# Kernel tuning notes

Measured on AMD Instinct MI355X. Metric: run time of the kernel, lower is better.

Reference implementation:

```python
import jax, jax.numpy as jnp
import numpy as np
import math

B, L, D, H = 2, 2048, 1024, 16
HD = D // H  # 64
SYNC_THRESHOLD = -0.7
LN_EPS = 1e-12


def setup_inputs() -> dict:
    key = jax.random.key(0)
    ks = jax.random.split(key, 12)
    s = 0.02
    return {
        "hidden_states": jax.random.normal(ks[0], (B, L, D), dtype=jnp.float32),
        "attention_mask": jnp.zeros((B, 1, 1, L), dtype=jnp.float32),
        "phi": jax.random.normal(ks[1], (B, L, H), dtype=jnp.float32),
        "Wq": jax.random.normal(ks[2], (D, D), dtype=jnp.float32) * s,
        "bq": jnp.zeros((D,), dtype=jnp.float32),
        "Wk": jax.random.normal(ks[3], (D, D), dtype=jnp.float32) * s,
        "bk": jnp.zeros((D,), dtype=jnp.float32),
        "Wv": jax.random.normal(ks[4], (D, D), dtype=jnp.float32) * s,
        "bv": jnp.zeros((D,), dtype=jnp.float32),
        "Wo": jax.random.normal(ks[5], (D, D), dtype=jnp.float32) * s,
        "bo": jnp.zeros((D,), dtype=jnp.float32),
        "ln_g": jnp.ones((D,), dtype=jnp.float32),
        "ln_b": jnp.zeros((D,), dtype=jnp.float32),
    }


def _shape(x):  # [B,L,D] -> [B,H,L,HD]
    return x.reshape(B, L, H, HD).transpose(0, 2, 1, 3)


def _rotate_half(x):
    x1, x2 = jnp.split(x, 2, axis=-1)
    return jnp.concatenate([-x2, x1], axis=-1)


def reference(hidden_states, attention_mask, phi, Wq, bq, Wk, bk, Wv, bv, Wo, bo, ln_g, ln_b):
    residual = hidden_states
    q = _shape(hidden_states @ Wq.T + bq)
    k = _shape(hidden_states @ Wk.T + bk)
    v = _shape(hidden_states @ Wv.T + bv)

    # phase per (batch, head, token): [B,H,L,1]; constant across head_dim,
    # so cos/sin of the concatenated phase are the same scalar per token/head.
    p = jnp.transpose(phi, (0, 2, 1))[..., None]
    cos_p = jnp.cos(p)
    sin_p = jnp.sin(p)
    q_rot = q * cos_p + _rotate_half(q) * sin_p
    k_rot = k * cos_p + _rotate_half(k) * sin_p

    scores = jnp.einsum("bhqd,bhkd->bhqk", q_rot, k_rot) / math.sqrt(HD)

    # data-dependent sync mask: mask pairs whose phase difference is anti-synced
    delta_phi = p - jnp.swapaxes(p, -1, -2)           # [B,H,L,L]
    eye = jnp.eye(L, dtype=bool)[None, None]          # [1,1,L,L]
    sync_mask = (jnp.cos(delta_phi) < SYNC_THRESHOLD) & ~eye
    scores = jnp.where(sync_mask, -1e9, scores)
    scores = scores + attention_mask

    # all-masked edge case: zero diagonal score so softmax attends to self
    row_max = jnp.max(scores, axis=-1, keepdims=True)
    all_masked = row_max <= -1e8
    scores = jnp.where(all_masked & eye, 0.0, scores)

    probs = jax.nn.softmax(scores, axis=-1)
    ctx = jnp.einsum("bhqk,bhkd->bhqd", probs, v)
    ctx = ctx.transpose(0, 2, 1, 3).reshape(B, L, D)

    out = ctx @ Wo.T + bo
    x = out + residual
    mean = jnp.mean(x, axis=-1, keepdims=True)
    var = jnp.var(x, axis=-1, keepdims=True)
    return (x - mean) / jnp.sqrt(var + LN_EPS) * ln_g + ln_b
```

## Files before the change

### kernel.cpp

```cpp
#include <hip/hip_runtime.h>
#include <cmath>

#define BB 2
#define LL 2048
#define DD 1024
#define HH 16
#define HDD 64

typedef _Float16 v8h __attribute__((ext_vector_type(8)));
typedef _Float16 v4h __attribute__((ext_vector_type(4)));
typedef _Float16 v2h __attribute__((ext_vector_type(2)));
typedef float v4f __attribute__((ext_vector_type(4)));

#define LOG2E 1.44269504089f
#define NEGB  (-1.442695e9f)

#define GLD(gp, lp)                                                        \
  __builtin_amdgcn_global_load_lds(                                        \
      (const __attribute__((address_space(1))) void*)(gp),                 \
      (__attribute__((address_space(3))) void*)(lp), 16, 0, 0)

__global__ __launch_bounds__(256) void cvt_all(
    const float* __restrict__ hs, const float* __restrict__ wq,
    const float* __restrict__ wk, const float* __restrict__ wv,
    const float* __restrict__ wo, _Float16* __restrict__ hsh,
    _Float16* __restrict__ wqkvh, _Float16* __restrict__ woh)
{
  const int i = blockIdx.x * 256 + threadIdx.x;
  const float* s;
  _Float16* d;
  if (i < 1048576)      { s = hs + (size_t)i * 4;            d = hsh + (size_t)i * 4; }
  else if (i < 1310720) { int j = i - 1048576; s = wq + (size_t)j * 4; d = wqkvh + (size_t)j * 4; }
  else if (i < 1572864) { int j = i - 1310720; s = wk + (size_t)j * 4; d = wqkvh + 1048576 + (size_t)j * 4; }
  else if (i < 1835008) { int j = i - 1572864; s = wv + (size_t)j * 4; d = wqkvh + 2097152 + (size_t)j * 4; }
  else                  { int j = i - 1835008; s = wo + (size_t)j * 4; d = woh + (size_t)j * 4; }
  float4 v = *(const float4*)s;
  v4h o;
  o[0] = (_Float16)v.x; o[1] = (_Float16)v.y;
  o[2] = (_Float16)v.z; o[3] = (_Float16)v.w;
  *(v4h*)d = o;
}

__global__ __launch_bounds__(256) void csgen(
    const float* __restrict__ phi, const float* __restrict__ amk,
    unsigned* __restrict__ csh2, float* __restrict__ aml2)
{
  const int o = blockIdx.x * 256 + threadIdx.x;
  if (o < BB * LL) aml2[o] = amk[o] * LOG2E;
  const int l = o & 2047;
  const int h = (o >> 11) & 15;
  const int b = o >> 15;
  const float ph = phi[(b * 2048 + l) * 16 + h];
  v2h cs;
  cs[0] = (_Float16)cosf(ph);
  cs[1] = (_Float16)sinf(ph);
  csh2[o] = __builtin_bit_cast(unsigned, cs);
}

__device__ __forceinline__ void gemm_loop(
    const _Float16* __restrict__ A, const _Float16* __restrict__ W, const int K,
    const int m0, const int n0, const int tid, const int wave, const int lane,
    _Float16* As, _Float16* Bs, v4f acc[4][4])
{
  const int quad = lane >> 4;
  const int ql = lane & 15;
  const int wm = (wave >> 1) * 64;
  const int wn = (wave & 1) * 64;
  const int srow = tid >> 2;
  const int skof = (tid & 3) * 8;
  const _Float16* Ap = A + (size_t)(m0 + srow) * K + skof;
  const _Float16* Wp = W + (size_t)(n0 + srow) * K + skof;
  const size_t rstep = (size_t)64 * K;
  for (int k0 = 0; k0 < K; k0 += 32) {
    __syncthreads();
    GLD(Ap + k0,         As + tid * 8);
    GLD(Ap + rstep + k0, As + 2048 + tid * 8);
    GLD(Wp + k0,         Bs + tid * 8);
    GLD(Wp + rstep + k0, Bs + 2048 + tid * 8);
    __syncthreads();
    v8h af[4], bf[4];
#pragma unroll
    for (int mt = 0; mt < 4; ++mt)
      af[mt] = *(const v8h*)&As[(wm + mt * 16 + ql) * 32 + quad * 8];
#pragma unroll
    for (int nt = 0; nt < 4; ++nt)
      bf[nt] = *(const v8h*)&Bs[(wn + nt * 16 + ql) * 32 + quad * 8];
#pragma unroll
    for (int mt = 0; mt < 4; ++mt)
#pragma unroll
      for (int nt = 0; nt < 4; ++nt)
        acc[mt][nt] = __builtin_amdgcn_mfma_f32_16x16x32_f16(
            af[mt], bf[nt], acc[mt][nt], 0, 0, 0);
  }
}

__global__ __launch_bounds__(256) void gemm_qkv(
    const _Float16* __restrict__ A, const _Float16* __restrict__ W,
    const float* __restrict__ bqp, const float* __restrict__ bkp,
    const float* __restrict__ bvp, const unsigned* __restrict__ csh2,
    _Float16* __restrict__ qh, _Float16* __restrict__ kh,
    _Float16* __restrict__ vt2)
{
  __shared__ _Float16 As[128 * 32];
  __shared__ _Float16 Bs[128 * 32];
  const int tid = threadIdx.x, lane = tid & 63, wave = tid >> 6;
  const int quad = lane >> 4, ql = lane & 15;
  const int m0 = blockIdx.y * 128, n0 = blockIdx.x * 128;
  v4f acc[4][4];
#pragma unroll
  for (int mt = 0; mt < 4; ++mt)
#pragma unroll
    for (int nt = 0; nt < 4; ++nt) acc[mt][nt] = (v4f){0.f, 0.f, 0.f, 0.f};
  gemm_loop(A, W, DD, m0, n0, tid, wave, lane, As, Bs, acc);

  const int buf = n0 >> 10;
  const int col0 = (n0 & 1023) + (wave & 1) * 64;
  const int hh = col0 >> 6;
  const int mr0 = m0 + (wave >> 1) * 64;

  if (buf == 2) {
    float bb4[4];
#pragma unroll
    for (int nt = 0; nt < 4; ++nt) bb4[nt] = bvp[col0 + nt * 16 + ql];
#pragma unroll
    for (int mt = 0; mt < 4; ++mt) {
      const int row = mr0 + mt * 16 + quad * 4;
      const int b_ = row >> 11;
      const int l = row & 2047;
      _Float16* dst = vt2 + ((size_t)(b_ * 16 + hh) * 32 + (l >> 6)) * 4096 +
                      ((l >> 2) & 15) * 256;
#pragma unroll
      for (int nt = 0; nt < 4; ++nt) {
        const int d = nt * 16 + ql;
        v4h o4;
#pragma unroll
        for (int r = 0; r < 4; ++r) o4[r] = (_Float16)(acc[mt][nt][r] + bb4[nt]);
        *(v4h*)&dst[d * 4] = o4;
      }
    }
  } else {
    const float scl = (buf == 0) ? 0.125f * LOG2E : 1.0f;
    _Float16* outp = (buf == 0) ? qh : kh;
    const float* bias = (buf == 0) ? bqp : bkp;
    float bb4[4];
#pragma unroll
    for (int nt = 0; nt < 4; ++nt) bb4[nt] = bias[col0 + nt * 16 + ql];
#pragma unroll
    for (int mt = 0; mt < 4; ++mt)
#pragma unroll
      for (int r = 0; r < 4; ++r) {
        const int row = mr0 + mt * 16 + quad * 4 + r;
        const int b_ = row >> 11;
        const int l = row & 2047;
        const v2h c2 = __builtin_bit_cast(
            v2h, csh2[(b_ * 16 + hh) * 2048 + l]);
        const float c = (float)c2[0], s = (float)c2[1];
        _Float16* orow = outp + (size_t)row * DD + col0 + ql;
#pragma unroll
        for (int pp = 0; pp < 2; ++pp) {
          const float a0 = acc[mt][pp][r] + bb4[pp];
          const float a1 = acc[mt][pp + 2][r] + bb4[pp + 2];
          orow[pp * 16]        = (_Float16)((a0 * c - a1 * s) * scl);
          orow[(pp + 2) * 16]  = (_Float16)((a1 * c + a0 * s) * scl);
        }
      }
  }
}

__global__ __launch_bounds__(256) void gemm_o(
    const _Float16* __restrict__ A, const _Float16* __restrict__ W,
    const float* __restrict__ bo, const float* __restrict__ res,
    float* __restrict__ out)
{
  __shared__ _Float16 As[128 * 32];
  __shared__ _Float16 Bs[64 * 32];
  const int tid = threadIdx.x, lane = tid & 63, wave = tid >> 6;
  const int quad = lane >> 4, ql = lane & 15;
  const int m0 = blockIdx.y * 128, n0 = blockIdx.x * 64;
  v4f acc[4][2];
#pragma unroll
  for (int mt = 0; mt < 4; ++mt)
#pragma unroll
    for (int nt = 0; nt < 2; ++nt) acc[mt][nt] = (v4f){0.f, 0.f, 0.f, 0.f};
  const int wm = (wave >> 1) * 64;
  const int wn = (wave & 1) * 32;
  const int srow = tid >> 2;
  const int skof = (tid & 3) * 8;
  const _Float16* Ap = A + (size_t)(m0 + srow) * DD + skof;
  const _Float16* Wp = W + (size_t)(n0 + srow) * DD + skof;
  const size_t rstep = (size_t)64 * DD;
  for (int k0 = 0; k0 < DD; k0 += 32) {
    __syncthreads();
    GLD(Ap + k0,         As + tid * 8);
    GLD(Ap + rstep + k0, As + 2048 + tid * 8);
    GLD(Wp + k0,         Bs + tid * 8);
    __syncthreads();
    v8h af[4], bf[2];
#pragma unroll
    for (int mt = 0; mt < 4; ++mt)
      af[mt] = *(const v8h*)&As[(wm + mt * 16 + ql) * 32 + quad * 8];
#pragma unroll
    for (int nt = 0; nt < 2; ++nt)
      bf[nt] = *(const v8h*)&Bs[(wn + nt * 16 + ql) * 32 + quad * 8];
#pragma unroll
    for (int mt = 0; mt < 4; ++mt)
#pragma unroll
      for (int nt = 0; nt < 2; ++nt)
        acc[mt][nt] = __builtin_amdgcn_mfma_f32_16x16x32_f16(
            af[mt], bf[nt], acc[mt][nt], 0, 0, 0);
  }
#pragma unroll
  for (int nt = 0; nt < 2; ++nt) {
    const int col = n0 + wn + nt * 16 + ql;
    const float bb = bo[col];
#pragma unroll
    for (int mt = 0; mt < 4; ++mt)
#pragma unroll
      for (int r = 0; r < 4; ++r) {
        const int row = m0 + wm + mt * 16 + quad * 4 + r;
        const size_t ix = (size_t)row * DD + col;
        out[ix] = acc[mt][nt][r] + bb + res[ix];
      }
  }
}

__global__ __launch_bounds__(256) void attn_db(
    const _Float16* __restrict__ Q, const _Float16* __restrict__ K,
    const _Float16* __restrict__ VT2, const unsigned* __restrict__ csh2,
    const float* __restrict__ aml2, _Float16* __restrict__ ctx)
{
  __shared__ _Float16 Kt[2][4096];
  __shared__ _Float16 Vt[2][4096];
  __shared__ float amL[LL];

  const int tid  = threadIdx.x;
  const int lane = tid & 63;
  const int wave = tid >> 6;
  const int quad = lane >> 4;
  const int ql   = lane & 15;
  const int bid  = blockIdx.x;
  const int bh = bid & 31;
  const int qt = bid >> 5;
  const int h  = bh & 15;
  const int b  = bh >> 4;
  const int q0w = qt * 64 + wave * 16;
  const int qglob = q0w + ql;
  const int csb = bh * LL;

  {
    const float* amb = aml2 + b * LL;
    for (int i = tid; i < LL; i += 256) amL[i] = amb[i];
  }

  v8h qf[2];
  {
    const _Float16* qp = Q + ((size_t)(b * LL + qglob)) * DD + h * 64 + quad * 8;
    qf[0] = *(const v8h*)qp;
    qf[1] = *(const v8h*)(qp + 32);
  }
  v4h bq = (v4h){0, 0, 0, 0};
  {
    const v2h c2 = __builtin_bit_cast(v2h, csh2[csb + qglob]);
    if (quad == 0) { bq[0] = c2[0]; bq[1] = c2[1]; }
  }
  const v4h ones = (v4h){(_Float16)1.f, (_Float16)1.f,
                         (_Float16)1.f, (_Float16)1.f};

  v4f o[4];
#pragma unroll
  for (int nt = 0; nt < 4; ++nt) o[nt] = (v4f){0.f, 0.f, 0.f, 0.f};
  v4f lacc = (v4f){0.f, 0.f, 0.f, 0.f};

  const _Float16* Kb   = K + (size_t)(b * LL) * DD + h * 64;
  const _Float16* VTb2 = VT2 + (size_t)bh * 131072;
  const unsigned* csk = csh2 + csb;

  const int srow = tid >> 3;
  const int kch  = (tid & 7) ^ (srow & 7);

  {
    const size_t kg = (size_t)srow * 1024 + kch * 8;
    GLD(Kb + kg,             &Kt[0][tid * 8]);
    GLD(Kb + kg + 32 * 1024, &Kt[0][2048 + tid * 8]);
    GLD(VTb2 + tid * 8,          &Vt[0][tid * 8]);
    GLD(VTb2 + 2048 + tid * 8,   &Vt[0][2048 + tid * 8]);
  }
  unsigned cs_cur[4], cs_nxt[4];
#pragma unroll
  for (int c = 0; c < 4; ++c) cs_cur[c] = csk[c * 16 + ql];
  __syncthreads();

  for (int t = 0; t < 32; ++t) {
    const int k0 = t * 64;
    const int buf = t & 1;
    if (t < 31) {
      const int k1 = k0 + 64;
      const size_t kg = (size_t)(k1 + srow) * 1024 + kch * 8;
      GLD(Kb + kg,             &Kt[buf ^ 1][tid * 8]);
      GLD(Kb + kg + 32 * 1024, &Kt[buf ^ 1][2048 + tid * 8]);
      const _Float16* vsrc = VTb2 + (size_t)(t + 1) * 4096;
      GLD(vsrc + tid * 8,        &Vt[buf ^ 1][tid * 8]);
      GLD(vsrc + 2048 + tid * 8, &Vt[buf ^ 1][2048 + tid * 8]);
#pragma unroll
      for (int c = 0; c < 4; ++c) cs_nxt[c] = csk[k1 + c * 16 + ql];
    }
    const _Float16* KtB = Kt[buf];
    const _Float16* VtB = Vt[buf];

    v4f st[4], dd[4];
#pragma unroll
    for (int c = 0; c < 4; ++c) {
      const int row = c * 16 + ql;
      const int sw = row & 7;
      v8h a0 = *(const v8h*)&KtB[row * 64 + ((quad ^ sw) << 3)];
      v8h a1 = *(const v8h*)&KtB[row * 64 + (((quad + 4) ^ sw) << 3)];
      v4f z = *(const v4f*)&amL[k0 + c * 16 + quad * 4];
      z = __builtin_amdgcn_mfma_f32_16x16x32_f16(a0, qf[0], z, 0, 0, 0);
      z = __builtin_amdgcn_mfma_f32_16x16x32_f16(a1, qf[1], z, 0, 0, 0);
      st[c] = z;
      const v2h c2 = __builtin_bit_cast(v2h, cs_cur[c]);
      v4h a = (v4h){0, 0, 0, 0};
      if (quad == 0) { a[0] = c2[0]; a[1] = c2[1]; }
      dd[c] = __builtin_amdgcn_mfma_f32_16x16x16f16(
          a, bq, (v4f){0.f, 0.f, 0.f, 0.f}, 0, 0, 0);
    }

    v4h pf[4];
#pragma unroll
    for (int c = 0; c < 4; ++c) {
      float p[4];
#pragma unroll
      for (int r = 0; r < 4; ++r)
        p[r] = __builtin_amdgcn_exp2f((dd[c][r] < -0.7f) ? NEGB : st[c][r]);
      const unsigned u01 = __builtin_bit_cast(
          unsigned, __builtin_amdgcn_cvt_pkrtz(p[0], p[1]));
      const unsigned u23 = __builtin_bit_cast(
          unsigned, __builtin_amdgcn_cvt_pkrtz(p[2], p[3]));
      pf[c] = __builtin_bit_cast(v4h, make_uint2(u01, u23));
    }

#pragma unroll
    for (int c = 0; c < 4; ++c) {
      lacc = __builtin_amdgcn_mfma_f32_16x16x16f16(pf[c], ones, lacc, 0, 0, 0);
#pragma unroll
      for (int nt = 0; nt < 4; ++nt) {
        const v4h vv = *(const v4h*)&VtB[((c * 4 + quad) * 64 +
                                          nt * 16 + ql) * 4];
        o[nt] = __builtin_amdgcn_mfma_f32_16x16x16f16(pf[c], vv, o[nt], 0, 0, 0);
      }
    }
#pragma unroll
    for (int c = 0; c < 4; ++c) cs_cur[c] = cs_nxt[c];
    __syncthreads();
  }

#pragma unroll
  for (int r = 0; r < 4; ++r) {
    const int q = q0w + quad * 4 + r;
    const float lr = lacc[r];
    const size_t ob = (size_t)(b * LL + q) * DD + h * 64 + ql;
    if (lr <= 0.f) {
      const _Float16* vsrc = VTb2 + (q >> 6) * 4096 +
                             ((q >> 2) & 15) * 256 + (q & 3);
#pragma unroll
      for (int nt = 0; nt < 4; ++nt)
        ctx[ob + nt * 16] = vsrc[(nt * 16 + ql) * 4];
    } else {
      const float inv = 1.f / lr;
      ctx[ob + 0]  = (_Float16)(o[0][r] * inv);
      ctx[ob + 16] = (_Float16)(o[1][r] * inv);
      ctx[ob + 32] = (_Float16)(o[2][r] * inv);
      ctx[ob + 48] = (_Float16)(o[3][r] * inv);
    }
  }
}

__global__ __launch_bounds__(256) void layernorm(
    const float* __restrict__ x, const float* __restrict__ g,
    const float* __restrict__ bta, float* __restrict__ out)
{
  __shared__ float red[8];
  const int row = blockIdx.x;
  const int tid = threadIdx.x;
  const float* xr = x + (size_t)row * DD;
  float lsum = 0.f, lsq = 0.f;
  float v[4];
#pragma unroll
  for (int i = 0; i < 4; ++i) {
    v[i] = xr[tid + i * 256];
    lsum += v[i];
    lsq += v[i] * v[i];
  }
#pragma unroll
  for (int off = 32; off > 0; off >>= 1) {
    lsum += __shfl_down(lsum, off, 64);
    lsq  += __shfl_down(lsq,  off, 64);
  }
  const int wid = tid >> 6;
  if ((tid & 63) == 0) { red[wid] = lsum; red[wid + 4] = lsq; }
  __syncthreads();
  const float tsum = red[0] + red[1] + red[2] + red[3];
  const float tsq  = red[4] + red[5] + red[6] + red[7];
  const float mean = tsum * (1.f / DD);
  const float var  = tsq * (1.f / DD) - mean * mean;
  const float inv  = rsqrtf(var + 1e-12f);
#pragma unroll
  for (int i = 0; i < 4; ++i) {
    const int c = tid + i * 256;
    out[(size_t)row * DD + c] = (v[i] - mean) * inv * g[c] + bta[c];
  }
}

extern "C" void kernel_launch(void* const* d_in, const int* in_sizes, int n_in,
                              void* d_out, int out_size, void* d_ws, size_t ws_size,
                              hipStream_t stream)
{
  const float* hs  = (const float*)d_in[0];
  const float* amk = (const float*)d_in[1];
  const float* phi = (const float*)d_in[2];
  const float* Wq  = (const float*)d_in[3];
  const float* bq  = (const float*)d_in[4];
  const float* Wk  = (const float*)d_in[5];
  const float* bk  = (const float*)d_in[6];
  const float* Wv  = (const float*)d_in[7];
  const float* bv  = (const float*)d_in[8];
  const float* Wo  = (const float*)d_in[9];
  const float* bo  = (const float*)d_in[10];
  const float* lng = (const float*)d_in[11];
  const float* lnb = (const float*)d_in[12];
  float* out = (float*)d_out;

  const size_t SZ = (size_t)BB * LL * DD;
  _Float16* hsh   = (_Float16*)d_ws;
  _Float16* qh    = hsh + SZ;
  _Float16* kh    = qh + SZ;
  _Float16* vt2   = kh + SZ;
  _Float16* ctxh  = vt2 + SZ;
  _Float16* wqkvh = ctxh + SZ;
  _Float16* woh   = wqkvh + 3 * (size_t)DD * DD;
  float* xb    = (float*)(woh + (size_t)DD * DD);
  unsigned* csh2 = (unsigned*)(xb + SZ);
  float* aml2 = (float*)(csh2 + (size_t)BB * HH * LL);

  cvt_all<<<8192, 256, 0, stream>>>(hs, Wq, Wk, Wv, Wo, hsh, wqkvh, woh);
  csgen<<<256, 256, 0, stream>>>(phi, amk, csh2, aml2);
  gemm_qkv<<<dim3(24, 32), 256, 0, stream>>>(hsh, wqkvh, bq, bk, bv, csh2,
                                             qh, kh, vt2);
  attn_db<<<1024, 256, 0, stream>>>(qh, kh, vt2, csh2, aml2, ctxh);
  gemm_o<<<dim3(16, 32), 256, 0, stream>>>(ctxh, woh, bo, hs, xb);
  layernorm<<<BB * LL, 256, 0, stream>>>(xb, lng, lnb, out);
}
```

Baseline: 240.3 us.

## Process two query tiles per wave in attention to reuse K/V tiles

```diff
diff --git a/kernel.cpp b/kernel.cpp
--- a/kernel.cpp
+++ b/kernel.cpp
@@ -224,7 +224,7 @@
   }
 }
 
-__global__ __launch_bounds__(256) void attn_db(
+__global__ __launch_bounds__(256, 2) void attn_db(
     const _Float16* __restrict__ Q, const _Float16* __restrict__ K,
     const _Float16* __restrict__ VT2, const unsigned* __restrict__ csh2,
     const float* __restrict__ aml2, _Float16* __restrict__ ctx)
@@ -243,8 +243,7 @@
   const int qt = bid >> 5;
   const int h  = bh & 15;
   const int b  = bh >> 4;
-  const int q0w = qt * 64 + wave * 16;
-  const int qglob = q0w + ql;
+  const int q0w = qt * 128 + wave * 32;
   const int csb = bh * LL;
 
   {
@@ -252,24 +251,37 @@
     for (int i = tid; i < LL; i += 256) amL[i] = amb[i];
   }
 
-  v8h qf[2];
+  v8h qf0[2], qf1[2];
+  v4h bq0, bq1;
   {
-    const _Float16* qp = Q + ((size_t)(b * LL + qglob)) * DD + h * 64 + quad * 8;
-    qf[0] = *(const v8h*)qp;
-    qf[1] = *(const v8h*)(qp + 32);
-  }
-  v4h bq = (v4h){0, 0, 0, 0};
+    const _Float16* qp = Q + ((size_t)(b * LL + q0w + ql)) * DD + h * 64 + quad * 8;
+    qf0[0] = *(const v8h*)qp;
+    qf0[1] = *(const v8h*)(qp + 32);
+    const v2h c2 = __builtin_bit_cast(v2h, csh2[csb + q0w + ql]);
+    v4h t = (v4h){0, 0, 0, 0};
+    if (quad == 0) { t[0] = c2[0]; t[1] = c2[1]; }
+    bq0 = t;
+  }
   {
-    const v2h c2 = __builtin_bit_cast(v2h, csh2[csb + qglob]);
-    if (quad == 0) { bq[0] = c2[0]; bq[1] = c2[1]; }
+    const _Float16* qp = Q + ((size_t)(b * LL + q0w + 16 + ql)) * DD + h * 64 + quad * 8;
+    qf1[0] = *(const v8h*)qp;
+    qf1[1] = *(const v8h*)(qp + 32);
+    const v2h c2 = __builtin_bit_cast(v2h, csh2[csb + q0w + 16 + ql]);
+    v4h t = (v4h){0, 0, 0, 0};
+    if (quad == 0) { t[0] = c2[0]; t[1] = c2[1]; }
+    bq1 = t;
   }
   const v4h ones = (v4h){(_Float16)1.f, (_Float16)1.f,
                          (_Float16)1.f, (_Float16)1.f};
 
-  v4f o[4];
-#pragma unroll
-  for (int nt = 0; nt < 4; ++nt) o[nt] = (v4f){0.f, 0.f, 0.f, 0.f};
-  v4f lacc = (v4f){0.f, 0.f, 0.f, 0.f};
+  v4f o0[4], o1[4];
+#pragma unroll
+  for (int nt = 0; nt < 4; ++nt) {
+    o0[nt] = (v4f){0.f, 0.f, 0.f, 0.f};
+    o1[nt] = (v4f){0.f, 0.f, 0.f, 0.f};
+  }
+  v4f lacc0 = (v4f){0.f, 0.f, 0.f, 0.f};
+  v4f lacc1 = (v4f){0.f, 0.f, 0.f, 0.f};
 
   const _Float16* Kb   = K + (size_t)(b * LL) * DD + h * 64;
   const _Float16* VTb2 = VT2 + (size_t)bh * 131072;
@@ -307,46 +319,64 @@
     const _Float16* KtB = Kt[buf];
     const _Float16* VtB = Vt[buf];
 
-    v4f st[4], dd[4];
+    v4f st0[4], st1[4], dd0[4], dd1[4];
 #pragma unroll
     for (int c = 0; c < 4; ++c) {
       const int row = c * 16 + ql;
       const int sw = row & 7;
       v8h a0 = *(const v8h*)&KtB[row * 64 + ((quad ^ sw) << 3)];
       v8h a1 = *(const v8h*)&KtB[row * 64 + (((quad + 4) ^ sw) << 3)];
-      v4f z = *(const v4f*)&amL[k0 + c * 16 + quad * 4];
-      z = __builtin_amdgcn_mfma_f32_16x16x32_f16(a0, qf[0], z, 0, 0, 0);
-      z = __builtin_amdgcn_mfma_f32_16x16x32_f16(a1, qf[1], z, 0, 0, 0);
-      st[c] = z;
+      v4f z0 = (v4f){0.f, 0.f, 0.f, 0.f};
+      z0 = __builtin_amdgcn_mfma_f32_16x16x32_f16(a0, qf0[0], z0, 0, 0, 0);
+      z0 = __builtin_amdgcn_mfma_f32_16x16x32_f16(a1, qf0[1], z0, 0, 0, 0);
+      st0[c] = z0;
+      v4f z1 = (v4f){0.f, 0.f, 0.f, 0.f};
+      z1 = __builtin_amdgcn_mfma_f32_16x16x32_f16(a0, qf1[0], z1, 0, 0, 0);
+      z1 = __builtin_amdgcn_mfma_f32_16x16x32_f16(a1, qf1[1], z1, 0, 0, 0);
+      st1[c] = z1;
       const v2h c2 = __builtin_bit_cast(v2h, cs_cur[c]);
       v4h a = (v4h){0, 0, 0, 0};
       if (quad == 0) { a[0] = c2[0]; a[1] = c2[1]; }
-      dd[c] = __builtin_amdgcn_mfma_f32_16x16x16f16(
-          a, bq, (v4f){0.f, 0.f, 0.f, 0.f}, 0, 0, 0);
-    }
-
-    v4h pf[4];
+      dd0[c] = __builtin_amdgcn_mfma_f32_16x16x16f16(
+          a, bq0, (v4f){0.f, 0.f, 0.f, 0.f}, 0, 0, 0);
+      dd1[c] = __builtin_amdgcn_mfma_f32_16x16x16f16(
+          a, bq1, (v4f){0.f, 0.f, 0.f, 0.f}, 0, 0, 0);
+    }
+
+    v4h pf0[4], pf1[4];
 #pragma unroll
     for (int c = 0; c < 4; ++c) {
-      float p[4];
-#pragma unroll
-      for (int r = 0; r < 4; ++r)
-        p[r] = __builtin_amdgcn_exp2f((dd[c][r] < -0.7f) ? NEGB : st[c][r]);
-      const unsigned u01 = __builtin_bit_cast(
-          unsigned, __builtin_amdgcn_cvt_pkrtz(p[0], p[1]));
-      const unsigned u23 = __builtin_bit_cast(
-          unsigned, __builtin_amdgcn_cvt_pkrtz(p[2], p[3]));
-      pf[c] = __builtin_bit_cast(v4h, make_uint2(u01, u23));
+      const v4f am4 = *(const v4f*)&amL[k0 + c * 16 + quad * 4];
+      float p0[4], p1[4];
+#pragma unroll
+      for (int r = 0; r < 4; ++r) {
+        p0[r] = __builtin_amdgcn_exp2f(
+            ((dd0[c][r] < -0.7f) ? NEGB : st0[c][r]) + am4[r]);
+        p1[r] = __builtin_amdgcn_exp2f(
+            ((dd1[c][r] < -0.7f) ? NEGB : st1[c][r]) + am4[r]);
+      }
+      const unsigned a01 = __builtin_bit_cast(
+          unsigned, __builtin_amdgcn_cvt_pkrtz(p0[0], p0[1]));
+      const unsigned a23 = __builtin_bit_cast(
+          unsigned, __builtin_amdgcn_cvt_pkrtz(p0[2], p0[3]));
+      pf0[c] = __builtin_bit_cast(v4h, make_uint2(a01, a23));
+      const unsigned b01 = __builtin_bit_cast(
+          unsigned, __builtin_amdgcn_cvt_pkrtz(p1[0], p1[1]));
+      const unsigned b23 = __builtin_bit_cast(
+          unsigned, __builtin_amdgcn_cvt_pkrtz(p1[2], p1[3]));
+      pf1[c] = __builtin_bit_cast(v4h, make_uint2(b01, b23));
     }
 
 #pragma unroll
     for (int c = 0; c < 4; ++c) {
-      lacc = __builtin_amdgcn_mfma_f32_16x16x16f16(pf[c], ones, lacc, 0, 0, 0);
+      lacc0 = __builtin_amdgcn_mfma_f32_16x16x16f16(pf0[c], ones, lacc0, 0, 0, 0);
+      lacc1 = __builtin_amdgcn_mfma_f32_16x16x16f16(pf1[c], ones, lacc1, 0, 0, 0);
 #pragma unroll
       for (int nt = 0; nt < 4; ++nt) {
         const v4h vv = *(const v4h*)&VtB[((c * 4 + quad) * 64 +
                                           nt * 16 + ql) * 4];
-        o[nt] = __builtin_amdgcn_mfma_f32_16x16x16f16(pf[c], vv, o[nt], 0, 0, 0);
+        o0[nt] = __builtin_amdgcn_mfma_f32_16x16x16f16(pf0[c], vv, o0[nt], 0, 0, 0);
+        o1[nt] = __builtin_amdgcn_mfma_f32_16x16x16f16(pf1[c], vv, o1[nt], 0, 0, 0);
       }
     }
 #pragma unroll
@@ -355,22 +385,27 @@
   }
 
 #pragma unroll
-  for (int r = 0; r < 4; ++r) {
-    const int q = q0w + quad * 4 + r;
-    const float lr = lacc[r];
-    const size_t ob = (size_t)(b * LL + q) * DD + h * 64 + ql;
-    if (lr <= 0.f) {
-      const _Float16* vsrc = VTb2 + (q >> 6) * 4096 +
-                             ((q >> 2) & 15) * 256 + (q & 3);
-#pragma unroll
-      for (int nt = 0; nt < 4; ++nt)
-        ctx[ob + nt * 16] = vsrc[(nt * 16 + ql) * 4];
-    } else {
-      const float inv = 1.f / lr;
-      ctx[ob + 0]  = (_Float16)(o[0][r] * inv);
-      ctx[ob + 16] = (_Float16)(o[1][r] * inv);
-      ctx[ob + 32] = (_Float16)(o[2][r] * inv);
-      ctx[ob + 48] = (_Float16)(o[3][r] * inv);
+  for (int g = 0; g < 2; ++g) {
+    const v4f* op = g ? o1 : o0;
+    const v4f la = g ? lacc1 : lacc0;
+#pragma unroll
+    for (int r = 0; r < 4; ++r) {
+      const int q = q0w + g * 16 + quad * 4 + r;
+      const float lr = la[r];
+      const size_t ob = (size_t)(b * LL + q) * DD + h * 64 + ql;
+      if (lr <= 0.f) {
+        const _Float16* vsrc = VTb2 + (q >> 6) * 4096 +
+                               ((q >> 2) & 15) * 256 + (q & 3);
+#pragma unroll
+        for (int nt = 0; nt < 4; ++nt)
+          ctx[ob + nt * 16] = vsrc[(nt * 16 + ql) * 4];
+      } else {
+        const float inv = 1.f / lr;
+        ctx[ob + 0]  = (_Float16)(op[0][r] * inv);
+        ctx[ob + 16] = (_Float16)(op[1][r] * inv);
+        ctx[ob + 32] = (_Float16)(op[2][r] * inv);
+        ctx[ob + 48] = (_Float16)(op[3][r] * inv);
+      }
     }
   }
 }
@@ -446,7 +481,7 @@
   csgen<<<256, 256, 0, stream>>>(phi, amk, csh2, aml2);
   gemm_qkv<<<dim3(24, 32), 256, 0, stream>>>(hsh, wqkvh, bq, bk, bv, csh2,
                                              qh, kh, vt2);
-  attn_db<<<1024, 256, 0, stream>>>(qh, kh, vt2, csh2, aml2, ctxh);
+  attn_db<<<512, 256, 0, stream>>>(qh, kh, vt2, csh2, aml2, ctxh);
   gemm_o<<<dim3(16, 32), 256, 0, stream>>>(ctxh, woh, bo, hs, xb);
   layernorm<<<BB * LL, 256, 0, stream>>>(xb, lng, lnb, out);
 }
```

Measured after the change: 232.8 us. 1.03x faster.

## Process four query groups per wave in attention to reuse K/V tiles

Applied to the files above, without the earlier changes.

```diff
diff --git a/kernel.cpp b/kernel.cpp
--- a/kernel.cpp
+++ b/kernel.cpp
@@ -224,7 +224,7 @@
   }
 }
 
-__global__ __launch_bounds__(256) void attn_db(
+__global__ __launch_bounds__(256, 1) void attn_db(
     const _Float16* __restrict__ Q, const _Float16* __restrict__ K,
     const _Float16* __restrict__ VT2, const unsigned* __restrict__ csh2,
     const float* __restrict__ aml2, _Float16* __restrict__ ctx)
@@ -243,8 +243,7 @@
   const int qt = bid >> 5;
   const int h  = bh & 15;
   const int b  = bh >> 4;
-  const int q0w = qt * 64 + wave * 16;
-  const int qglob = q0w + ql;
+  const int q0w = qt * 256 + wave * 64;
   const int csb = bh * LL;
 
   {
@@ -252,24 +251,30 @@
     for (int i = tid; i < LL; i += 256) amL[i] = amb[i];
   }
 
-  v8h qf[2];
-  {
-    const _Float16* qp = Q + ((size_t)(b * LL + qglob)) * DD + h * 64 + quad * 8;
-    qf[0] = *(const v8h*)qp;
-    qf[1] = *(const v8h*)(qp + 32);
-  }
-  v4h bq = (v4h){0, 0, 0, 0};
-  {
-    const v2h c2 = __builtin_bit_cast(v2h, csh2[csb + qglob]);
-    if (quad == 0) { bq[0] = c2[0]; bq[1] = c2[1]; }
+  v8h qf[4][2];
+  v4h bq[4];
+#pragma unroll
+  for (int g = 0; g < 4; ++g) {
+    const int qg = q0w + g * 16 + ql;
+    const _Float16* qp = Q + ((size_t)(b * LL + qg)) * DD + h * 64 + quad * 8;
+    qf[g][0] = *(const v8h*)qp;
+    qf[g][1] = *(const v8h*)(qp + 32);
+    const v2h c2 = __builtin_bit_cast(v2h, csh2[csb + qg]);
+    v4h t = (v4h){0, 0, 0, 0};
+    if (quad == 0) { t[0] = c2[0]; t[1] = c2[1]; }
+    bq[g] = t;
   }
   const v4h ones = (v4h){(_Float16)1.f, (_Float16)1.f,
                          (_Float16)1.f, (_Float16)1.f};
 
-  v4f o[4];
-#pragma unroll
-  for (int nt = 0; nt < 4; ++nt) o[nt] = (v4f){0.f, 0.f, 0.f, 0.f};
-  v4f lacc = (v4f){0.f, 0.f, 0.f, 0.f};
+  v4f o[4][4];
+  v4f lacc[4];
+#pragma unroll
+  for (int g = 0; g < 4; ++g) {
+    lacc[g] = (v4f){0.f, 0.f, 0.f, 0.f};
+#pragma unroll
+    for (int nt = 0; nt < 4; ++nt) o[g][nt] = (v4f){0.f, 0.f, 0.f, 0.f};
+  }
 
   const _Float16* Kb   = K + (size_t)(b * LL) * DD + h * 64;
   const _Float16* VTb2 = VT2 + (size_t)bh * 131072;
@@ -307,46 +312,56 @@
     const _Float16* KtB = Kt[buf];
     const _Float16* VtB = Vt[buf];
 
-    v4f st[4], dd[4];
+    v4h pf[4][4];
 #pragma unroll
     for (int c = 0; c < 4; ++c) {
       const int row = c * 16 + ql;
       const int sw = row & 7;
       v8h a0 = *(const v8h*)&KtB[row * 64 + ((quad ^ sw) << 3)];
       v8h a1 = *(const v8h*)&KtB[row * 64 + (((quad + 4) ^ sw) << 3)];
-      v4f z = *(const v4f*)&amL[k0 + c * 16 + quad * 4];
-      z = __builtin_amdgcn_mfma_f32_16x16x32_f16(a0, qf[0], z, 0, 0, 0);
-      z = __builtin_amdgcn_mfma_f32_16x16x32_f16(a1, qf[1], z, 0, 0, 0);
-      st[c] = z;
       const v2h c2 = __builtin_bit_cast(v2h, cs_cur[c]);
       v4h a = (v4h){0, 0, 0, 0};
       if (quad == 0) { a[0] = c2[0]; a[1] = c2[1]; }
-      dd[c] = __builtin_amdgcn_mfma_f32_16x16x16f16(
-          a, bq, (v4f){0.f, 0.f, 0.f, 0.f}, 0, 0, 0);
+      const v4f am4 = *(const v4f*)&amL[k0 + c * 16 + quad * 4];
+      v4f st[4], dd[4];
+#pragma unroll
+      for (int g = 0; g < 4; ++g) {
+        v4f z = (v4f){0.f, 0.f, 0.f, 0.f};
+        z = __builtin_amdgcn_mfma_f32_16x16x32_f16(a0, qf[g][0], z, 0, 0, 0);
+        z = __builtin_amdgcn_mfma_f32_16x16x32_f16(a1, qf[g][1], z, 0, 0, 0);
+        st[g] = z;
+        dd[g] = __builtin_amdgcn_mfma_f32_16x16x16f16(
+            a, bq[g], (v4f){0.f, 0.f, 0.f, 0.f}, 0, 0, 0);
+      }
+#pragma unroll
+      for (int g = 0; g < 4; ++g) {
+        float p[4];
+#pragma unroll
+        for (int r = 0; r < 4; ++r)
+          p[r] = __builtin_amdgcn_exp2f(
+              ((dd[g][r] < -0.7f) ? NEGB : st[g][r]) + am4[r]);
+        const unsigned u01 = __builtin_bit_cast(
+            unsigned, __builtin_amdgcn_cvt_pkrtz(p[0], p[1]));
+        const unsigned u23 = __builtin_bit_cast(
+            unsigned, __builtin_amdgcn_cvt_pkrtz(p[2], p[3]));
+        pf[c][g] = __builtin_bit_cast(v4h, make_uint2(u01, u23));
+      }
     }
 
-    v4h pf[4];
 #pragma unroll
     for (int c = 0; c < 4; ++c) {
-      float p[4];
-#pragma unroll
-      for (int r = 0; r < 4; ++r)
-        p[r] = __builtin_amdgcn_exp2f((dd[c][r] < -0.7f) ? NEGB : st[c][r]);
-      const unsigned u01 = __builtin_bit_cast(
-          unsigned, __builtin_amdgcn_cvt_pkrtz(p[0], p[1]));
-      const unsigned u23 = __builtin_bit_cast(
-          unsigned, __builtin_amdgcn_cvt_pkrtz(p[2], p[3]));
-      pf[c] = __builtin_bit_cast(v4h, make_uint2(u01, u23));
-    }
-
-#pragma unroll
-    for (int c = 0; c < 4; ++c) {
-      lacc = __builtin_amdgcn_mfma_f32_16x16x16f16(pf[c], ones, lacc, 0, 0, 0);
+#pragma unroll
+      for (int g = 0; g < 4; ++g)
+        lacc[g] = __builtin_amdgcn_mfma_f32_16x16x16f16(
+            pf[c][g], ones, lacc[g], 0, 0, 0);
 #pragma unroll
       for (int nt = 0; nt < 4; ++nt) {
         const v4h vv = *(const v4h*)&VtB[((c * 4 + quad) * 64 +
                                           nt * 16 + ql) * 4];
-        o[nt] = __builtin_amdgcn_mfma_f32_16x16x16f16(pf[c], vv, o[nt], 0, 0, 0);
+#pragma unroll
+        for (int g = 0; g < 4; ++g)
+          o[g][nt] = __builtin_amdgcn_mfma_f32_16x16x16f16(
+              pf[c][g], vv, o[g][nt], 0, 0, 0);
       }
     }
 #pragma unroll
@@ -355,22 +370,25 @@
   }
 
 #pragma unroll
-  for (int r = 0; r < 4; ++r) {
-    const int q = q0w + quad * 4 + r;
-    const float lr = lacc[r];
-    const size_t ob = (size_t)(b * LL + q) * DD + h * 64 + ql;
-    if (lr <= 0.f) {
-      const _Float16* vsrc = VTb2 + (q >> 6) * 4096 +
-                             ((q >> 2) & 15) * 256 + (q & 3);
-#pragma unroll
-      for (int nt = 0; nt < 4; ++nt)
-        ctx[ob + nt * 16] = vsrc[(nt * 16 + ql) * 4];
-    } else {
-      const float inv = 1.f / lr;
-      ctx[ob + 0]  = (_Float16)(o[0][r] * inv);
-      ctx[ob + 16] = (_Float16)(o[1][r] * inv);
-      ctx[ob + 32] = (_Float16)(o[2][r] * inv);
-      ctx[ob + 48] = (_Float16)(o[3][r] * inv);
+  for (int g = 0; g < 4; ++g) {
+#pragma unroll
+    for (int r = 0; r < 4; ++r) {
+      const int q = q0w + g * 16 + quad * 4 + r;
+      const float lr = lacc[g][r];
+      const size_t ob = (size_t)(b * LL + q) * DD + h * 64 + ql;
+      if (lr <= 0.f) {
+        const _Float16* vsrc = VTb2 + (q >> 6) * 4096 +
+                               ((q >> 2) & 15) * 256 + (q & 3);
+#pragma unroll
+        for (int nt = 0; nt < 4; ++nt)
+          ctx[ob + nt * 16] = vsrc[(nt * 16 + ql) * 4];
+      } else {
+        const float inv = 1.f / lr;
+        ctx[ob + 0]  = (_Float16)(o[g][0][r] * inv);
+        ctx[ob + 16] = (_Float16)(o[g][1][r] * inv);
+        ctx[ob + 32] = (_Float16)(o[g][2][r] * inv);
+        ctx[ob + 48] = (_Float16)(o[g][3][r] * inv);
+      }
     }
   }
 }
@@ -446,7 +464,7 @@
   csgen<<<256, 256, 0, stream>>>(phi, amk, csh2, aml2);
   gemm_qkv<<<dim3(24, 32), 256, 0, stream>>>(hsh, wqkvh, bq, bk, bv, csh2,
                                              qh, kh, vt2);
-  attn_db<<<1024, 256, 0, stream>>>(qh, kh, vt2, csh2, aml2, ctxh);
+  attn_db<<<256, 256, 0, stream>>>(qh, kh, vt2, csh2, aml2, ctxh);
   gemm_o<<<dim3(16, 32), 256, 0, stream>>>(ctxh, woh, bo, hs, xb);
   layernorm<<<BB * LL, 256, 0, stream>>>(xb, lng, lnb, out);
 }
```

Result: slower. 267.8 us (+11.5%).
